# Optimization experiments

Hardware: AMD Instinct MI355X
Metric: run time of the kernel (lower is better)

The kernel has to match this reference:

```python
import jax, jax.numpy as jnp
import numpy as np

N = 50000
E = 640000
F_IN = 128
HID = 128
OUT = 64


def setup_inputs() -> dict:
    key = jax.random.key(0)
    ks = jax.random.split(key, 16)
    x = jax.random.normal(ks[0], (N, F_IN), dtype=jnp.float32)
    edge_index = jax.random.randint(ks[1], (2, E), 0, N, dtype=jnp.int64)

    def lin(k, fan_in, fan_out):
        bound = 1.0 / np.sqrt(fan_in)
        kw, kb = jax.random.split(k)
        W = jax.random.uniform(kw, (fan_in, fan_out), jnp.float32, -bound, bound)
        b = jax.random.uniform(kb, (fan_out,), jnp.float32, -bound, bound)
        return W, b

    W1, b1 = lin(ks[2], F_IN, HID)
    W2, b2 = lin(ks[3], HID, HID)
    W3, b3 = lin(ks[4], HID, HID)
    Wres, bres = lin(ks[5], F_IN, HID)
    Wlin, blin = lin(ks[6], HID, OUT)
    return {"x": x, "edge_index": edge_index,
            "W1": W1, "b1": b1, "W2": W2, "b2": b2, "W3": W3, "b3": b3,
            "Wres": Wres, "bres": bres, "Wlin": Wlin, "blin": blin}


def _gcn_norm(edge_index, n):
    # GCNConv default: add self-loops, symmetric normalization D^-1/2 (A+I) D^-1/2
    src, dst = edge_index[0], edge_index[1]
    deg = jax.ops.segment_sum(jnp.ones((edge_index.shape[1],), jnp.float32), dst,
                              num_segments=n) + 1.0  # +1 for self-loop
    dinv = jax.lax.rsqrt(deg)
    norm_e = dinv[src] * dinv[dst]          # [E] edge coefficients
    norm_self = 1.0 / deg                    # [N] self-loop coefficients
    return src, dst, norm_e, norm_self


def _gcn_conv(x, W, b, src, dst, norm_e, norm_self, n):
    h = x @ W                                # [N, F_out]
    agg = jax.ops.segment_sum(h[src] * norm_e[:, None], dst, num_segments=n)
    agg = agg + h * norm_self[:, None]       # self-loop contribution
    return agg + b


def reference(x, edge_index, W1, b1, W2, b2, W3, b3, Wres, bres, Wlin, blin):
    n = x.shape[0]
    src, dst, norm_e, norm_self = _gcn_norm(edge_index, n)
    x_res = x @ Wres + bres
    h = _gcn_conv(x, W1, b1, src, dst, norm_e, norm_self, n)
    h = jax.nn.relu(h + x_res)               # dropout is identity in eval mode
    h = _gcn_conv(h, W2, b2, src, dst, norm_e, norm_self, n)
    h = jax.nn.relu(h)
    h = _gcn_conv(h, W3, b3, src, dst, norm_e, norm_self, n)
    h = jax.nn.relu(h)
    return h @ Wlin + blin
```

## Files before the change

### kernel.cpp

```cpp
#include <hip/hip_runtime.h>

typedef unsigned short ushort_t;
typedef unsigned int uint_t;

typedef __bf16 bf16x8 __attribute__((ext_vector_type(8)));
typedef float f32x4 __attribute__((ext_vector_type(4)));

union BFU { ushort_t u; __bf16 h; };

__device__ __forceinline__ float bf2f(uint_t u) {
    union { uint_t i; float f; } v; v.i = u << 16; return v.f;
}
__device__ __forceinline__ ushort_t f2bf(float f) {
    union { float f; uint_t i; } v; v.f = f;
    uint_t r = v.i + 0x7fffu + ((v.i >> 16) & 1u);
    return (ushort_t)(r >> 16);
}
__device__ __forceinline__ float loadF(const void* p, size_t i, int isBf16) {
    return isBf16 ? bf2f((uint_t)((const ushort_t*)p)[i]) : ((const float*)p)[i];
}

struct DetectArgs {
    const void* t[11];
    int elems[11];
    const int* ei;
    int* flags;
};

__device__ __forceinline__ int detect_one(const void* p, int elems) {
    const uint_t* w = (const uint_t*)p;
    int n = elems / 2; if (n > 64) n = 64;
    int cnt = 0;
    for (int k = 0; k < n; ++k) {
        uint_t f = (w[k] >> 7) & 0xFFu;
        cnt += (f >= 100u && f <= 135u);
    }
    return (cnt * 10 >= n * 6) ? 1 : 0;
}

__global__ void k_pack(DetectArgs a,
                       ushort_t* __restrict__ Tcat, ushort_t* __restrict__ T2,
                       ushort_t* __restrict__ T3, ushort_t* __restrict__ Tl,
                       int* __restrict__ deg, int N, uint_t* __restrict__ Hz) {
    __shared__ int lflag;
    int i = blockIdx.x * blockDim.x + threadIdx.x;
    if (i < N) deg[i] = 0;
    if (blockIdx.x == 1 && threadIdx.x < 64) Hz[threadIdx.x] = 0u;
    const int SQ = 128 * 128;
    int m = (i < 4 * SQ) ? (i / SQ) : 4;
    int fid = (m == 0) ? 1 : (m == 1) ? 3 : (m == 2) ? 5 : (m == 3) ? 7 : 9;
    const void* W = a.t[fid];

    if (threadIdx.x == 0) lflag = detect_one(W, a.elems[fid]);
    if (blockIdx.x == 0 && threadIdx.x >= 64 && threadIdx.x < 75) {
        int t = threadIdx.x - 64;
        a.flags[t] = detect_one(a.t[t], a.elems[t]);
    }
    if (blockIdx.x == 0 && threadIdx.x == 75) {
        int nz = 0;
        for (int k = 0; k < 64; ++k) nz += (a.ei[2 * k + 1] != 0);
        a.flags[11] = (nz == 0) ? 1 : 0;
    }
    __syncthreads();
    int isb = lflag;

    if (i < 4 * SQ) {
        int r = i % SQ;
        int k = r / 128, f = r % 128;
        ushort_t* T = (m == 0) ? Tcat : (m == 1) ? T2 : (m == 2) ? T3 : (Tcat + SQ);
        T[f * 128 + k] = f2bf(loadF(W, (size_t)k * 128 + f, isb));
    } else if (i < 4 * SQ + 128 * 64) {
        int r = i - 4 * SQ;
        int k = r / 64, f = r % 64;
        Tl[f * 128 + k] = f2bf(loadF(W, (size_t)k * 64 + f, isb));
    }
}

__global__ void k_deg(const int* __restrict__ ei, int E, int N,
                      const int* __restrict__ flags, int* __restrict__ deg,
                      int2* __restrict__ tmp) {
    int i = blockIdx.x * blockDim.x + threadIdx.x;
    int e0 = i * 4;
    if (e0 >= E) return;
    int is64 = flags[11];
    if (e0 + 3 < E && (E & 3) == 0) {
        int d[4];
        if (is64) {
            int4 va = *(const int4*)(ei + 2 * E + 2 * e0);
            int4 vb = *(const int4*)(ei + 2 * E + 2 * e0 + 4);
            d[0] = va.x; d[1] = va.z; d[2] = vb.x; d[3] = vb.z;
        } else {
            int4 va = *(const int4*)(ei + E + e0);
            d[0] = va.x; d[1] = va.y; d[2] = va.z; d[3] = va.w;
        }
        int l[4]; bool ok[4];
#pragma unroll
        for (int k = 0; k < 4; ++k) ok[k] = (unsigned)d[k] < (unsigned)N;
#pragma unroll
        for (int k = 0; k < 4; ++k)
            l[k] = ok[k] ? atomicAdd(&deg[d[k]], 1) : 0;
        int4 t01, t23;
        t01.x = ok[0] ? d[0] : -1; t01.y = l[0];
        t01.z = ok[1] ? d[1] : -1; t01.w = l[1];
        t23.x = ok[2] ? d[2] : -1; t23.y = l[2];
        t23.z = ok[3] ? d[3] : -1; t23.w = l[3];
        *(int4*)(tmp + e0) = t01;
        *(int4*)(tmp + e0 + 2) = t23;
    } else {
        for (int e = e0; e < E && e < e0 + 4; ++e) {
            int dd = is64 ? ei[2 * E + 2 * e] : ei[E + e];
            bool ok = (unsigned)dd < (unsigned)N;
            int l = ok ? atomicAdd(&deg[dd], 1) : 0;
            tmp[e] = make_int2(ok ? dd : -1, l);
        }
    }
}


__global__ __launch_bounds__(256) void k_bsum(const int* __restrict__ deg, int n,
                                              int* __restrict__ bsum) {
    int base = blockIdx.x * 1024;
    int local = 0;
#pragma unroll
    for (int j = 0; j < 4; ++j) {
        int idx = base + threadIdx.x + j * 256;
        if (idx < n) local += deg[idx];
    }
    __shared__ int s[4];
#pragma unroll
    for (int off = 32; off; off >>= 1) local += __shfl_down(local, off, 64);
    if ((threadIdx.x & 63) == 0) s[threadIdx.x >> 6] = local;
    __syncthreads();
    if (threadIdx.x == 0) bsum[blockIdx.x] = s[0] + s[1] + s[2] + s[3];
}

__global__ __launch_bounds__(256) void k_rowptr(const int* __restrict__ deg,
                                                const int* __restrict__ bsum, int n,
                                                int* __restrict__ row_ptr,
                                                float* __restrict__ dinv) {
    __shared__ int s[256];
    __shared__ int sboff;
    int t = threadIdx.x;

    if (t < 64) {
        int v = (t < blockIdx.x) ? bsum[t] : 0;
#pragma unroll
        for (int off = 32; off; off >>= 1) v += __shfl_down(v, off, 64);
        if (t == 0) sboff = v;
    }

    int base = blockIdx.x * 1024 + t * 4;
    int v0 = (base + 0 < n) ? deg[base + 0] : 0;
    int v1 = (base + 1 < n) ? deg[base + 1] : 0;
    int v2 = (base + 2 < n) ? deg[base + 2] : 0;
    int v3 = (base + 3 < n) ? deg[base + 3] : 0;
    int tot = v0 + v1 + v2 + v3;
    s[t] = tot;
    __syncthreads();
    for (int off = 1; off < 256; off <<= 1) {
        int u = (t >= off) ? s[t - off] : 0;
        __syncthreads();
        s[t] += u;
        __syncthreads();
    }
    int run = sboff + ((t == 0) ? 0 : s[t - 1]);
    int vals[4] = {v0, v1, v2, v3};
#pragma unroll
    for (int j = 0; j < 4; ++j) {
        int idx = base + j;
        if (idx < n) {
            row_ptr[idx] = run;
            run += vals[j];
            float df = (float)vals[j] + 1.0f;
            dinv[idx] = rsqrtf(df);
        }
    }
    if (blockIdx.x == gridDim.x - 1 && t == 255) row_ptr[n] = sboff + s[255];
}

__global__ void k_scatter(const int* __restrict__ ei, int E, int N,
                          const int* __restrict__ flags,
                          const int* __restrict__ row_ptr,
                          const int2* __restrict__ tmp,
                          uint_t* __restrict__ colw) {
    int i = blockIdx.x * blockDim.x + threadIdx.x;
    int e0 = i * 4;
    if (e0 >= E) return;
    int is64 = flags[11];
    if (e0 + 3 < E && (E & 3) == 0) {
        int s[4];
        if (is64) {
            int4 sa = *(const int4*)(ei + 2 * e0);
            int4 sb = *(const int4*)(ei + 2 * e0 + 4);
            s[0] = sa.x; s[1] = sa.z; s[2] = sb.x; s[3] = sb.z;
        } else {
            int4 sa = *(const int4*)(ei + e0);
            s[0] = sa.x; s[1] = sa.y; s[2] = sa.z; s[3] = sa.w;
        }
        int4 t01 = *(const int4*)(tmp + e0);
        int4 t23 = *(const int4*)(tmp + e0 + 2);
        int d[4] = {t01.x, t01.z, t23.x, t23.z};
        int l[4] = {t01.y, t01.w, t23.y, t23.w};
        int ss[4];
#pragma unroll
        for (int k = 0; k < 4; ++k)
            ss[k] = ((unsigned)s[k] < (unsigned)N) ? s[k] : 0;
#pragma unroll
        for (int k = 0; k < 4; ++k) {
            if (d[k] >= 0)
                colw[row_ptr[d[k]] + l[k]] = (uint_t)ss[k];
        }
    } else {
        for (int e = e0; e < E && e < e0 + 4; ++e) {
            int sv = is64 ? ei[2 * e] : ei[e];
            int2 tv = tmp[e];
            if (tv.x >= 0) {
                int ssv = ((unsigned)sv < (unsigned)N) ? sv : 0;
                colw[row_ptr[tv.x] + tv.y] = (uint_t)ssv;
            }
        }
    }
}


template <int NCT>
__device__ __forceinline__ void stage_B(const ushort_t* __restrict__ WT, uint4* lds) {
    int t = threadIdx.x;
#pragma unroll
    for (int i = 0; i < NCT; ++i) {
        int g = i * 256 + t;
        uint4 v = ((const uint4*)WT)[g];
        int col = g >> 4, k8 = g & 15;
        int c = col >> 4, l16c = col & 15;
        int kk = k8 >> 2, q = k8 & 3;
        lds[((kk * NCT + c) << 6) + (q << 4) + l16c] = v;
    }
    __syncthreads();
}

__device__ __forceinline__ void load_A1(const void* __restrict__ A, int a16,
                                        int ar, int quad, bf16x8 af[4]) {
    if (a16) {
        const ushort_t* p = (const ushort_t*)A + (size_t)ar * 128 + quad * 8;
#pragma unroll
        for (int kk = 0; kk < 4; ++kk) af[kk] = *(const bf16x8*)(p + kk * 32);
    } else {
        const float* p = (const float*)A + (size_t)ar * 128 + quad * 8;
#pragma unroll
        for (int kk = 0; kk < 4; ++kk) {
            f32x4 u0 = *(const f32x4*)(p + kk * 32);
            f32x4 u1 = *(const f32x4*)(p + kk * 32 + 4);
#pragma unroll
            for (int j = 0; j < 4; ++j) {
                BFU e;
                e.u = f2bf(u0[j]); af[kk][j] = e.h;
                e.u = f2bf(u1[j]); af[kk][j + 4] = e.h;
            }
        }
    }
}

template <int NCT>
__global__ __launch_bounds__(256, 4) void k_gemm2(const void* __restrict__ A, int aFid, int aFix,
                                                  const ushort_t* __restrict__ WT,
                                                  const void* __restrict__ bias, int bFid,
                                                  void* __restrict__ C, int cFix,
                                                  int M, const int* __restrict__ flags,
                                                  const float* __restrict__ rowscale) {
    __shared__ uint4 lds[NCT * 256];
    stage_B<NCT>(WT, lds);

    const int F = NCT * 16;
    int t = threadIdx.x;
    int wave = t >> 6, lane = t & 63;
    int quad = lane >> 4, l16 = lane & 15;
    int row0 = blockIdx.x * 64 + wave * 16;

    int a16 = (aFid >= 0) ? flags[aFid] : aFix;
    int ar = row0 + l16; if (ar >= M) ar = M - 1;

    bf16x8 af[4];
    load_A1(A, a16, ar, quad, af);

    f32x4 acc[NCT];
#pragma unroll
    for (int c = 0; c < NCT; ++c) acc[c] = (f32x4){0.f, 0.f, 0.f, 0.f};

#pragma unroll
    for (int kk = 0; kk < 4; ++kk) {
#pragma unroll
        for (int c = 0; c < NCT; ++c) {
            bf16x8 b = *(const bf16x8*)&lds[((kk * NCT + c) << 6) + lane];
            acc[c] = __builtin_amdgcn_mfma_f32_16x16x32_bf16(af[kk], b, acc[c], 0, 0, 0);
        }
    }

    float rs[4];
#pragma unroll
    for (int q = 0; q < 4; ++q) {
        int row = row0 + quad * 4 + q;
        rs[q] = (rowscale && row < M) ? rowscale[row] : 1.0f;
    }

    int bf = (bias && bFid >= 0) ? flags[bFid] : 1;
#pragma unroll
    for (int c = 0; c < NCT; ++c) {
        int colg = c * 16 + l16;
        float bv = bias ? loadF(bias, colg, bf) : 0.0f;
#pragma unroll
        for (int q = 0; q < 4; ++q) {
            int row = row0 + quad * 4 + q;
            if (row < M) {
                float v = acc[c][q] * rs[q] + bv;
                if (cFix) ((ushort_t*)C)[(size_t)row * F + colg] = f2bf(v);
                else      ((float*)C)[(size_t)row * F + colg] = v;
            }
        }
    }
}

__global__ __launch_bounds__(256, 4) void k_gemm_l1(const void* __restrict__ A,
                                                    const ushort_t* __restrict__ Tcat,
                                                    const void* __restrict__ bres,
                                                    ushort_t* __restrict__ Hout,
                                                    ushort_t* __restrict__ Xres,
                                                    int M, const int* __restrict__ flags,
                                                    const float* __restrict__ dinv) {
    __shared__ uint4 lds[8 * 256];
    int t = threadIdx.x;
    int wave = t >> 6, lane = t & 63;
    int quad = lane >> 4, l16 = lane & 15;
    int row0 = blockIdx.x * 64 + wave * 16;

    int a16 = flags[0];
    int ar = row0 + l16; if (ar >= M) ar = M - 1;

    bf16x8 af[4];
    load_A1(A, a16, ar, quad, af);

    float rs[4];
#pragma unroll
    for (int q = 0; q < 4; ++q) {
        int row = row0 + quad * 4 + q;
        rs[q] = (row < M) ? dinv[row] : 1.0f;
    }

    stage_B<8>(Tcat, lds);
    {
        f32x4 acc[8];
#pragma unroll
        for (int c = 0; c < 8; ++c) acc[c] = (f32x4){0.f, 0.f, 0.f, 0.f};
#pragma unroll
        for (int kk = 0; kk < 4; ++kk) {
#pragma unroll
            for (int c = 0; c < 8; ++c) {
                bf16x8 b = *(const bf16x8*)&lds[((kk * 8 + c) << 6) + lane];
                acc[c] = __builtin_amdgcn_mfma_f32_16x16x32_bf16(af[kk], b, acc[c], 0, 0, 0);
            }
        }
#pragma unroll
        for (int c = 0; c < 8; ++c) {
            int colg = c * 16 + l16;
#pragma unroll
            for (int q = 0; q < 4; ++q) {
                int row = row0 + quad * 4 + q;
                if (row < M) Hout[(size_t)row * 128 + colg] = f2bf(acc[c][q] * rs[q]);
            }
        }
    }
    __syncthreads();

    stage_B<8>(Tcat + 128 * 128, lds);
    {
        int bf = flags[8];
        f32x4 acc[8];
#pragma unroll
        for (int c = 0; c < 8; ++c) acc[c] = (f32x4){0.f, 0.f, 0.f, 0.f};
#pragma unroll
        for (int kk = 0; kk < 4; ++kk) {
#pragma unroll
            for (int c = 0; c < 8; ++c) {
                bf16x8 b = *(const bf16x8*)&lds[((kk * 8 + c) << 6) + lane];
                acc[c] = __builtin_amdgcn_mfma_f32_16x16x32_bf16(af[kk], b, acc[c], 0, 0, 0);
            }
        }
#pragma unroll
        for (int c = 0; c < 8; ++c) {
            int colg = c * 16 + l16;
            float bv = loadF(bres, colg, bf);
#pragma unroll
            for (int q = 0; q < 4; ++q) {
                int row = row0 + quad * 4 + q;
                if (row < M) Xres[(size_t)row * 128 + colg] = f2bf(acc[c][q] + bv);
            }
        }
    }
}

__global__ __launch_bounds__(256) void k_agg(const ushort_t* __restrict__ H,
                                             const int* __restrict__ row_ptr,
                                             const uint_t* __restrict__ colw,
                                             const float* __restrict__ dinv,
                                             const void* __restrict__ bias, int bFid,
                                             const ushort_t* __restrict__ other,
                                             ushort_t* __restrict__ Out,
                                             int n, const int* __restrict__ flags) {
    int node = (blockIdx.x * blockDim.x + threadIdx.x) >> 6;
    if (node >= n) return;
    int lane = threadIdx.x & 63;
    int f = lane * 2;

    size_t nidx = (size_t)node * 128 + f;

    uint_t hv = *(const uint_t*)(H + nidx);
    float a0 = bf2f(hv & 0xffffu);
    float a1 = bf2f(hv >> 16);

    int beg = row_ptr[node], end = row_ptr[node + 1];
    for (int bs = beg; bs < end; bs += 64) {
        int rem = end - bs;
        int nb = (rem < 64) ? rem : 64;
        int c = (lane < nb) ? (int)colw[bs + lane] : n;

        for (int j = 0; j < nb; j += 16) {
            int si[16]; uint_t vi[16];
#pragma unroll
            for (int q = 0; q < 16; ++q) si[q] = __shfl(c, j + q, 64);
#pragma unroll
            for (int q = 0; q < 16; ++q)
                vi[q] = *(const uint_t*)(H + (size_t)si[q] * 128 + f);
#pragma unroll
            for (int q = 0; q < 16; ++q) {
                a0 += bf2f(vi[q] & 0xffffu);
                a1 += bf2f(vi[q] >> 16);
            }
        }
    }

    float dv = dinv[node];
    int bfm = flags[bFid];
    float a0o = fmaf(a0, dv, loadF(bias, f, bfm));
    float a1o = fmaf(a1, dv, loadF(bias, f + 1, bfm));
    if (other) {
        uint_t ov = *(const uint_t*)(other + nidx);
        a0o += bf2f(ov & 0xffffu);
        a1o += bf2f(ov >> 16);
    }
    a0o = fmaxf(a0o, 0.0f);
    a1o = fmaxf(a1o, 0.0f);
    *(uint_t*)(Out + nidx) = (uint_t)f2bf(a0o) | ((uint_t)f2bf(a1o) << 16);
}


extern "C" void kernel_launch(void* const* d_in, const int* in_sizes, int n_in,
                              void* d_out, int out_size, void* d_ws, size_t ws_size,
                              hipStream_t stream) {
    const int N = in_sizes[0] / 128;
    const int E = in_sizes[1] / 2;

    const void* x  = d_in[0];
    const int*  ei = (const int*)d_in[1];

    char* ws = (char*)d_ws;
    size_t used = 0;
    auto alloc = [&](size_t bytes) {
        char* p = ws + used;
        used += (bytes + 255) & ~(size_t)255;
        return p;
    };

    int*   flags   = (int*)alloc(64 * 4);
    int*   deg     = (int*)alloc((size_t)N * 4);
    int*   row_ptr = (int*)alloc((size_t)(N + 1) * 4);
    float* dinv    = (float*)alloc((size_t)N * 4);
    int2*  tmp     = (int2*)alloc((size_t)E * 8);
    uint_t* colw   = (uint_t*)alloc((size_t)E * 4);
    int*   bsum    = (int*)alloc(256 * 4);
    ushort_t* Tcat = (ushort_t*)alloc(256 * 128 * 2);
    ushort_t* T2   = (ushort_t*)alloc(128 * 128 * 2);
    ushort_t* T3   = (ushort_t*)alloc(128 * 128 * 2);
    ushort_t* Tlin = (ushort_t*)alloc(128 * 64 * 2);

    ushort_t* Hbuf = (ushort_t*)alloc((size_t)(N + 1) * 128 * 2);
    ushort_t* Act1 = (ushort_t*)alloc((size_t)N * 128 * 2);
    ushort_t* Act2 = (ushort_t*)alloc((size_t)N * 128 * 2);
    ushort_t* Xres = (ushort_t*)alloc((size_t)N * 128 * 2);

    if (used > ws_size) return;

    DetectArgs da;
    for (int i = 0; i < 11; ++i) { da.t[i] = d_in[i == 0 ? 0 : i + 1]; da.elems[i] = in_sizes[i == 0 ? 0 : i + 1]; }
    da.ei = ei;
    da.flags = flags;

    const int B = 256;
    int gE4   = ((E + 3) / 4 + B - 1) / B;
    int gPack = (4 * 128 * 128 + 128 * 64) / B;
    int gGemm = (N + 63) / 64;
    int gAgg  = (N + 3) / 4;
    int nb    = (N + 1023) / 1024;

    uint_t* Hz = (uint_t*)(Hbuf + (size_t)N * 128);

    k_pack<<<gPack, B, 0, stream>>>(da, Tcat, T2, T3, Tlin, deg, N, Hz);
    k_deg<<<gE4, B, 0, stream>>>(ei, E, N, flags, deg, tmp);
    k_bsum<<<nb, B, 0, stream>>>(deg, N, bsum);
    k_rowptr<<<nb, B, 0, stream>>>(deg, bsum, N, row_ptr, dinv);
    k_scatter<<<gE4, B, 0, stream>>>(ei, E, N, flags, row_ptr, tmp, colw);

    k_gemm_l1<<<gGemm, B, 0, stream>>>(x, Tcat, d_in[9], Hbuf, Xres, N, flags, dinv);
    k_agg<<<gAgg, B, 0, stream>>>(Hbuf, row_ptr, colw, dinv, d_in[3], 2,
                                  Xres, Act1, N, flags);

    k_gemm2<8><<<gGemm, B, 0, stream>>>(Act1, -1, 1, T2, nullptr, -1, Hbuf, 1, N, flags, dinv);
    k_agg<<<gAgg, B, 0, stream>>>(Hbuf, row_ptr, colw, dinv, d_in[5], 4,
                                  nullptr, Act2, N, flags);

    k_gemm2<8><<<gGemm, B, 0, stream>>>(Act2, -1, 1, T3, nullptr, -1, Hbuf, 1, N, flags, dinv);
    k_agg<<<gAgg, B, 0, stream>>>(Hbuf, row_ptr, colw, dinv, d_in[7], 6,
                                  nullptr, Act1, N, flags);

    k_gemm2<4><<<gGemm, B, 0, stream>>>(Act1, -1, 1, Tlin, d_in[11], 10,
                                        d_out, 0, N, flags, nullptr);
}
```

Measured before the change: 284.2 us.

## Split aggregation features across four blocks and edges across wave quarters

The aggregation kernel now gives each node's 128 features to four blocks of 32 features each. Within a wave, each quarter processes a different subset of the neighbors, and the partial sums are combined with xor shuffles. Index loads, residual loads and output stores use nontemporal hints. The aim is more parallelism and shorter per-wave dependency chains on low-degree nodes, at the cost of four times as many blocks and narrower 64-byte gather segments per row.

```diff
diff --git a/kernel.cpp b/kernel.cpp
--- a/kernel.cpp
+++ b/kernel.cpp
@@ -405,50 +405,59 @@
                                              const ushort_t* __restrict__ other,
                                              ushort_t* __restrict__ Out,
                                              int n, const int* __restrict__ flags) {
-    int node = (blockIdx.x * blockDim.x + threadIdx.x) >> 6;
+    int s = blockIdx.x & 3;
+    int node = (blockIdx.x >> 2) * 4 + (threadIdx.x >> 6);
     if (node >= n) return;
     int lane = threadIdx.x & 63;
-    int f = lane * 2;
-
+    int e4 = lane >> 4;
+    int fl = lane & 15;
+    int f = s * 32 + fl * 2;
     size_t nidx = (size_t)node * 128 + f;
 
-    uint_t hv = *(const uint_t*)(H + nidx);
-    float a0 = bf2f(hv & 0xffffu);
-    float a1 = bf2f(hv >> 16);
-
     int beg = row_ptr[node], end = row_ptr[node + 1];
+    float a0 = 0.f, a1 = 0.f;
+
     for (int bs = beg; bs < end; bs += 64) {
         int rem = end - bs;
         int nb = (rem < 64) ? rem : 64;
-        int c = (lane < nb) ? (int)colw[bs + lane] : n;
+        int c = (lane < nb) ? (int)__builtin_nontemporal_load(&colw[bs + lane]) : n;
 
         for (int j = 0; j < nb; j += 16) {
-            int si[16]; uint_t vi[16];
-#pragma unroll
-            for (int q = 0; q < 16; ++q) si[q] = __shfl(c, j + q, 64);
-#pragma unroll
-            for (int q = 0; q < 16; ++q)
-                vi[q] = *(const uint_t*)(H + (size_t)si[q] * 128 + f);
-#pragma unroll
-            for (int q = 0; q < 16; ++q) {
-                a0 += bf2f(vi[q] & 0xffffu);
-                a1 += bf2f(vi[q] >> 16);
-            }
-        }
-    }
-
-    float dv = dinv[node];
-    int bfm = flags[bFid];
-    float a0o = fmaf(a0, dv, loadF(bias, f, bfm));
-    float a1o = fmaf(a1, dv, loadF(bias, f + 1, bfm));
-    if (other) {
-        uint_t ov = *(const uint_t*)(other + nidx);
-        a0o += bf2f(ov & 0xffffu);
-        a1o += bf2f(ov >> 16);
-    }
-    a0o = fmaxf(a0o, 0.0f);
-    a1o = fmaxf(a1o, 0.0f);
-    *(uint_t*)(Out + nidx) = (uint_t)f2bf(a0o) | ((uint_t)f2bf(a1o) << 16);
+            int ce[4]; uint_t v[4];
+#pragma unroll
+            for (int q = 0; q < 4; ++q) ce[q] = __shfl(c, j + q * 4 + e4, 64);
+#pragma unroll
+            for (int q = 0; q < 4; ++q)
+                v[q] = *(const uint_t*)(H + (size_t)ce[q] * 128 + f);
+#pragma unroll
+            for (int q = 0; q < 4; ++q) {
+                a0 += bf2f(v[q] & 0xffffu);
+                a1 += bf2f(v[q] >> 16);
+            }
+        }
+    }
+
+    a0 += __shfl_xor(a0, 16, 64); a1 += __shfl_xor(a1, 16, 64);
+    a0 += __shfl_xor(a0, 32, 64); a1 += __shfl_xor(a1, 32, 64);
+
+    if (e4 == 0) {
+        uint_t hv = *(const uint_t*)(H + nidx);
+        a0 += bf2f(hv & 0xffffu);
+        a1 += bf2f(hv >> 16);
+        float dv = dinv[node];
+        int bfm = flags[bFid];
+        float a0o = fmaf(a0, dv, loadF(bias, f, bfm));
+        float a1o = fmaf(a1, dv, loadF(bias, f + 1, bfm));
+        if (other) {
+            uint_t ov = __builtin_nontemporal_load((const uint_t*)(other + nidx));
+            a0o += bf2f(ov & 0xffffu);
+            a1o += bf2f(ov >> 16);
+        }
+        a0o = fmaxf(a0o, 0.0f);
+        a1o = fmaxf(a1o, 0.0f);
+        __builtin_nontemporal_store((uint_t)f2bf(a0o) | ((uint_t)f2bf(a1o) << 16),
+                                    (uint_t*)(Out + nidx));
+    }
 }
 
 
@@ -497,7 +506,7 @@
     int gE4   = ((E + 3) / 4 + B - 1) / B;
     int gPack = (4 * 128 * 128 + 128 * 64) / B;
     int gGemm = (N + 63) / 64;
-    int gAgg  = (N + 3) / 4;
+    int gAgg  = ((N + 3) / 4) * 4;
     int nb    = (N + 1023) / 1024;
 
     uint_t* Hz = (uint_t*)(Hbuf + (size_t)N * 128);
```

After: 422.0 us. +48.5%, slower.

## Fuse neighbor aggregation with following GEMM via LDS-staged activation tiles

Applied to the files above, without the earlier changes.

Merges each aggregation kernel with the next layer's dense GEMM. Each wave aggregates 16 nodes serially, writes the bf16 activations into an LDS tile, then runs MFMA against the staged weights. The bf16 activation round trip through global memory and three launches go away, and ping-pong H buffers get zeroed padding rows. In exchange the grid drops from one wave per node to one wave per 16 nodes, which cuts parallelism for the latency-bound gather, and occupancy falls with the extra LDS and the launch bound lowered to 3.

```diff
diff --git a/kernel.cpp b/kernel.cpp
--- a/kernel.cpp
+++ b/kernel.cpp
@@ -41,11 +41,15 @@
 __global__ void k_pack(DetectArgs a,
                        ushort_t* __restrict__ Tcat, ushort_t* __restrict__ T2,
                        ushort_t* __restrict__ T3, ushort_t* __restrict__ Tl,
-                       int* __restrict__ deg, int N, uint_t* __restrict__ Hz) {
+                       int* __restrict__ deg, int N,
+                       uint_t* __restrict__ HzA, uint_t* __restrict__ HzB) {
     __shared__ int lflag;
     int i = blockIdx.x * blockDim.x + threadIdx.x;
     if (i < N) deg[i] = 0;
-    if (blockIdx.x == 1 && threadIdx.x < 64) Hz[threadIdx.x] = 0u;
+    if (blockIdx.x == 1 && threadIdx.x < 128) {
+        uint_t* Hz = (threadIdx.x < 64) ? HzA : HzB;
+        Hz[threadIdx.x & 63] = 0u;
+    }
     const int SQ = 128 * 128;
     int m = (i < 4 * SQ) ? (i / SQ) : 4;
     int fid = (m == 0) ? 1 : (m == 1) ? 3 : (m == 2) ? 5 : (m == 3) ? 7 : 9;
@@ -260,65 +264,6 @@
     }
 }
 
-template <int NCT>
-__global__ __launch_bounds__(256, 4) void k_gemm2(const void* __restrict__ A, int aFid, int aFix,
-                                                  const ushort_t* __restrict__ WT,
-                                                  const void* __restrict__ bias, int bFid,
-                                                  void* __restrict__ C, int cFix,
-                                                  int M, const int* __restrict__ flags,
-                                                  const float* __restrict__ rowscale) {
-    __shared__ uint4 lds[NCT * 256];
-    stage_B<NCT>(WT, lds);
-
-    const int F = NCT * 16;
-    int t = threadIdx.x;
-    int wave = t >> 6, lane = t & 63;
-    int quad = lane >> 4, l16 = lane & 15;
-    int row0 = blockIdx.x * 64 + wave * 16;
-
-    int a16 = (aFid >= 0) ? flags[aFid] : aFix;
-    int ar = row0 + l16; if (ar >= M) ar = M - 1;
-
-    bf16x8 af[4];
-    load_A1(A, a16, ar, quad, af);
-
-    f32x4 acc[NCT];
-#pragma unroll
-    for (int c = 0; c < NCT; ++c) acc[c] = (f32x4){0.f, 0.f, 0.f, 0.f};
-
-#pragma unroll
-    for (int kk = 0; kk < 4; ++kk) {
-#pragma unroll
-        for (int c = 0; c < NCT; ++c) {
-            bf16x8 b = *(const bf16x8*)&lds[((kk * NCT + c) << 6) + lane];
-            acc[c] = __builtin_amdgcn_mfma_f32_16x16x32_bf16(af[kk], b, acc[c], 0, 0, 0);
-        }
-    }
-
-    float rs[4];
-#pragma unroll
-    for (int q = 0; q < 4; ++q) {
-        int row = row0 + quad * 4 + q;
-        rs[q] = (rowscale && row < M) ? rowscale[row] : 1.0f;
-    }
-
-    int bf = (bias && bFid >= 0) ? flags[bFid] : 1;
-#pragma unroll
-    for (int c = 0; c < NCT; ++c) {
-        int colg = c * 16 + l16;
-        float bv = bias ? loadF(bias, colg, bf) : 0.0f;
-#pragma unroll
-        for (int q = 0; q < 4; ++q) {
-            int row = row0 + quad * 4 + q;
-            if (row < M) {
-                float v = acc[c][q] * rs[q] + bv;
-                if (cFix) ((ushort_t*)C)[(size_t)row * F + colg] = f2bf(v);
-                else      ((float*)C)[(size_t)row * F + colg] = v;
-            }
-        }
-    }
-}
-
 __global__ __launch_bounds__(256, 4) void k_gemm_l1(const void* __restrict__ A,
                                                     const ushort_t* __restrict__ Tcat,
                                                     const void* __restrict__ bres,
@@ -397,58 +342,123 @@
     }
 }
 
-__global__ __launch_bounds__(256) void k_agg(const ushort_t* __restrict__ H,
-                                             const int* __restrict__ row_ptr,
-                                             const uint_t* __restrict__ colw,
-                                             const float* __restrict__ dinv,
-                                             const void* __restrict__ bias, int bFid,
-                                             const ushort_t* __restrict__ other,
-                                             ushort_t* __restrict__ Out,
-                                             int n, const int* __restrict__ flags) {
-    int node = (blockIdx.x * blockDim.x + threadIdx.x) >> 6;
-    if (node >= n) return;
-    int lane = threadIdx.x & 63;
+template <int NCT, int CF32>
+__global__ __launch_bounds__(256, 3) void k_fused(const ushort_t* __restrict__ H,
+                                                  const int* __restrict__ row_ptr,
+                                                  const uint_t* __restrict__ colw,
+                                                  const float* __restrict__ dinv,
+                                                  const void* __restrict__ bagg, int baggFid,
+                                                  const ushort_t* __restrict__ other,
+                                                  const ushort_t* __restrict__ WT,
+                                                  const void* __restrict__ bgemm, int bgFid,
+                                                  void* __restrict__ C,
+                                                  int n, const int* __restrict__ flags) {
+    __shared__ uint4 lds_w[NCT * 256];
+    __shared__ uint_t lds_act[4 * 16 * 68];
+
+    stage_B<NCT>(WT, lds_w);
+
+    int t = threadIdx.x;
+    int wave = t >> 6, lane = t & 63;
     int f = lane * 2;
-
-    size_t nidx = (size_t)node * 128 + f;
-
-    uint_t hv = *(const uint_t*)(H + nidx);
-    float a0 = bf2f(hv & 0xffffu);
-    float a1 = bf2f(hv >> 16);
-
-    int beg = row_ptr[node], end = row_ptr[node + 1];
-    for (int bs = beg; bs < end; bs += 64) {
-        int rem = end - bs;
-        int nb = (rem < 64) ? rem : 64;
-        int c = (lane < nb) ? (int)colw[bs + lane] : n;
-
-        for (int j = 0; j < nb; j += 16) {
-            int si[16]; uint_t vi[16];
-#pragma unroll
-            for (int q = 0; q < 16; ++q) si[q] = __shfl(c, j + q, 64);
-#pragma unroll
-            for (int q = 0; q < 16; ++q)
-                vi[q] = *(const uint_t*)(H + (size_t)si[q] * 128 + f);
-#pragma unroll
-            for (int q = 0; q < 16; ++q) {
-                a0 += bf2f(vi[q] & 0xffffu);
-                a1 += bf2f(vi[q] >> 16);
-            }
-        }
-    }
-
-    float dv = dinv[node];
-    int bfm = flags[bFid];
-    float a0o = fmaf(a0, dv, loadF(bias, f, bfm));
-    float a1o = fmaf(a1, dv, loadF(bias, f + 1, bfm));
-    if (other) {
-        uint_t ov = *(const uint_t*)(other + nidx);
-        a0o += bf2f(ov & 0xffffu);
-        a1o += bf2f(ov >> 16);
-    }
-    a0o = fmaxf(a0o, 0.0f);
-    a1o = fmaxf(a1o, 0.0f);
-    *(uint_t*)(Out + nidx) = (uint_t)f2bf(a0o) | ((uint_t)f2bf(a1o) << 16);
+    int row0 = blockIdx.x * 64 + wave * 16;
+    uint_t* act = lds_act + wave * (16 * 68);
+    int bfm = flags[baggFid];
+
+    for (int i = 0; i < 16; ++i) {
+        int node = row0 + i;
+        int nd = (node < n) ? node : (n - 1);
+        int beg = row_ptr[nd], end = row_ptr[nd + 1];
+
+        uint_t hv = *(const uint_t*)(H + (size_t)nd * 128 + f);
+        float a0 = bf2f(hv & 0xffffu);
+        float a1 = bf2f(hv >> 16);
+
+        for (int bs = beg; bs < end; bs += 64) {
+            int rem = end - bs;
+            int nb = (rem < 64) ? rem : 64;
+            int c = (lane < nb) ? (int)colw[bs + lane] : n;
+
+            for (int j = 0; j < nb; j += 16) {
+                int si[16]; uint_t vi[16];
+#pragma unroll
+                for (int q = 0; q < 16; ++q) si[q] = __shfl(c, j + q, 64);
+#pragma unroll
+                for (int q = 0; q < 16; ++q)
+                    vi[q] = *(const uint_t*)(H + (size_t)si[q] * 128 + f);
+#pragma unroll
+                for (int q = 0; q < 16; ++q) {
+                    a0 += bf2f(vi[q] & 0xffffu);
+                    a1 += bf2f(vi[q] >> 16);
+                }
+            }
+        }
+
+        float dv = dinv[nd];
+        float a0o = fmaf(a0, dv, loadF(bagg, f, bfm));
+        float a1o = fmaf(a1, dv, loadF(bagg, f + 1, bfm));
+        if (other) {
+            uint_t ov = *(const uint_t*)(other + (size_t)nd * 128 + f);
+            a0o += bf2f(ov & 0xffffu);
+            a1o += bf2f(ov >> 16);
+        }
+        a0o = fmaxf(a0o, 0.0f);
+        a1o = fmaxf(a1o, 0.0f);
+        act[i * 68 + lane] = (uint_t)f2bf(a0o) | ((uint_t)f2bf(a1o) << 16);
+    }
+
+    int quad = lane >> 4, l16 = lane & 15;
+
+    bf16x8 af[4];
+#pragma unroll
+    for (int kk = 0; kk < 4; ++kk)
+        af[kk] = *(const bf16x8*)&act[l16 * 68 + kk * 16 + quad * 4];
+
+    f32x4 acc[NCT];
+#pragma unroll
+    for (int c = 0; c < NCT; ++c) acc[c] = (f32x4){0.f, 0.f, 0.f, 0.f};
+
+#pragma unroll
+    for (int kk = 0; kk < 4; ++kk) {
+#pragma unroll
+        for (int c = 0; c < NCT; ++c) {
+            bf16x8 b = *(const bf16x8*)&lds_w[((kk * NCT + c) << 6) + lane];
+            acc[c] = __builtin_amdgcn_mfma_f32_16x16x32_bf16(af[kk], b, acc[c], 0, 0, 0);
+        }
+    }
+
+    const int F = NCT * 16;
+    if (CF32) {
+        int bg = (bgemm) ? flags[bgFid] : 1;
+#pragma unroll
+        for (int c = 0; c < NCT; ++c) {
+            int colg = c * 16 + l16;
+            float bv = bgemm ? loadF(bgemm, colg, bg) : 0.0f;
+#pragma unroll
+            for (int q = 0; q < 4; ++q) {
+                int row = row0 + quad * 4 + q;
+                if (row < n)
+                    ((float*)C)[(size_t)row * F + colg] = acc[c][q] + bv;
+            }
+        }
+    } else {
+        float rs[4];
+#pragma unroll
+        for (int q = 0; q < 4; ++q) {
+            int row = row0 + quad * 4 + q;
+            rs[q] = (row < n) ? dinv[row] : 1.0f;
+        }
+#pragma unroll
+        for (int c = 0; c < NCT; ++c) {
+            int colg = c * 16 + l16;
+#pragma unroll
+            for (int q = 0; q < 4; ++q) {
+                int row = row0 + quad * 4 + q;
+                if (row < n)
+                    ((ushort_t*)C)[(size_t)row * F + colg] = f2bf(acc[c][q] * rs[q]);
+            }
+        }
+    }
 }
 
 
@@ -481,9 +491,8 @@
     ushort_t* T3   = (ushort_t*)alloc(128 * 128 * 2);
     ushort_t* Tlin = (ushort_t*)alloc(128 * 64 * 2);
 
-    ushort_t* Hbuf = (ushort_t*)alloc((size_t)(N + 1) * 128 * 2);
-    ushort_t* Act1 = (ushort_t*)alloc((size_t)N * 128 * 2);
-    ushort_t* Act2 = (ushort_t*)alloc((size_t)N * 128 * 2);
+    ushort_t* Ha   = (ushort_t*)alloc((size_t)(N + 1) * 128 * 2);
+    ushort_t* Hb   = (ushort_t*)alloc((size_t)(N + 1) * 128 * 2);
     ushort_t* Xres = (ushort_t*)alloc((size_t)N * 128 * 2);
 
     if (used > ws_size) return;
@@ -497,29 +506,25 @@
     int gE4   = ((E + 3) / 4 + B - 1) / B;
     int gPack = (4 * 128 * 128 + 128 * 64) / B;
     int gGemm = (N + 63) / 64;
-    int gAgg  = (N + 3) / 4;
     int nb    = (N + 1023) / 1024;
 
-    uint_t* Hz = (uint_t*)(Hbuf + (size_t)N * 128);
-
-    k_pack<<<gPack, B, 0, stream>>>(da, Tcat, T2, T3, Tlin, deg, N, Hz);
+    uint_t* HzA = (uint_t*)(Ha + (size_t)N * 128);
+    uint_t* HzB = (uint_t*)(Hb + (size_t)N * 128);
+
+    k_pack<<<gPack, B, 0, stream>>>(da, Tcat, T2, T3, Tlin, deg, N, HzA, HzB);
     k_deg<<<gE4, B, 0, stream>>>(ei, E, N, flags, deg, tmp);
     k_bsum<<<nb, B, 0, stream>>>(deg, N, bsum);
     k_rowptr<<<nb, B, 0, stream>>>(deg, bsum, N, row_ptr, dinv);
     k_scatter<<<gE4, B, 0, stream>>>(ei, E, N, flags, row_ptr, tmp, colw);
 
-    k_gemm_l1<<<gGemm, B, 0, stream>>>(x, Tcat, d_in[9], Hbuf, Xres, N, flags, dinv);
-    k_agg<<<gAgg, B, 0, stream>>>(Hbuf, row_ptr, colw, dinv, d_in[3], 2,
-                                  Xres, Act1, N, flags);
-
-    k_gemm2<8><<<gGemm, B, 0, stream>>>(Act1, -1, 1, T2, nullptr, -1, Hbuf, 1, N, flags, dinv);
-    k_agg<<<gAgg, B, 0, stream>>>(Hbuf, row_ptr, colw, dinv, d_in[5], 4,
-                                  nullptr, Act2, N, flags);
-
-    k_gemm2<8><<<gGemm, B, 0, stream>>>(Act2, -1, 1, T3, nullptr, -1, Hbuf, 1, N, flags, dinv);
-    k_agg<<<gAgg, B, 0, stream>>>(Hbuf, row_ptr, colw, dinv, d_in[7], 6,
-                                  nullptr, Act1, N, flags);
-
-    k_gemm2<4><<<gGemm, B, 0, stream>>>(Act1, -1, 1, Tlin, d_in[11], 10,
-                                        d_out, 0, N, flags, nullptr);
-}
+    k_gemm_l1<<<gGemm, B, 0, stream>>>(x, Tcat, d_in[9], Ha, Xres, N, flags, dinv);
+
+    k_fused<8, 0><<<gGemm, B, 0, stream>>>(Ha, row_ptr, colw, dinv, d_in[3], 2,
+                                           Xres, T2, nullptr, -1, Hb, N, flags);
+
+    k_fused<8, 0><<<gGemm, B, 0, stream>>>(Hb, row_ptr, colw, dinv, d_in[5], 4,
+                                           nullptr, T3, nullptr, -1, Ha, N, flags);
+
+    k_fused<4, 1><<<gGemm, B, 0, stream>>>(Ha, row_ptr, colw, dinv, d_in[7], 6,
+                                           nullptr, Tlin, d_in[11], 10, d_out, N, flags);
+}
```

Result: slower. 348.6 us (+22.7%).

## Split each aggregation wave into two half-waves gathering different neighbors with wider loads

Applied to the files above, without the earlier changes.

Restructures the CSR gather so each 64-lane wave handles two neighbor rows at once: each 32-lane half loads 4 bf16 features (8 bytes) per lane for alternating neighbors, and the halves are combined with a cross-half shuffle at the end. Neighbor indices are read as wave-uniform scalar loads of 16 at a time instead of a per-lane load plus shuffles. The goal is to raise memory-level parallelism and cut shuffle overhead in the bandwidth-bound gather. The column buffer is padded so the 16-wide index reads past the end stay in bounds, and for low-degree nodes some slots point at a dummy row n, which adds wasted loads.

```diff
diff --git a/kernel.cpp b/kernel.cpp
--- a/kernel.cpp
+++ b/kernel.cpp
@@ -408,47 +408,68 @@
     int node = (blockIdx.x * blockDim.x + threadIdx.x) >> 6;
     if (node >= n) return;
     int lane = threadIdx.x & 63;
-    int f = lane * 2;
-
-    size_t nidx = (size_t)node * 128 + f;
-
-    uint_t hv = *(const uint_t*)(H + nidx);
-    float a0 = bf2f(hv & 0xffffu);
-    float a1 = bf2f(hv >> 16);
-
-    int beg = row_ptr[node], end = row_ptr[node + 1];
-    for (int bs = beg; bs < end; bs += 64) {
-        int rem = end - bs;
-        int nb = (rem < 64) ? rem : 64;
-        int c = (lane < nb) ? (int)colw[bs + lane] : n;
-
-        for (int j = 0; j < nb; j += 16) {
-            int si[16]; uint_t vi[16];
-#pragma unroll
-            for (int q = 0; q < 16; ++q) si[q] = __shfl(c, j + q, 64);
-#pragma unroll
-            for (int q = 0; q < 16; ++q)
-                vi[q] = *(const uint_t*)(H + (size_t)si[q] * 128 + f);
-#pragma unroll
-            for (int q = 0; q < 16; ++q) {
-                a0 += bf2f(vi[q] & 0xffffu);
-                a1 += bf2f(vi[q] >> 16);
-            }
-        }
-    }
-
-    float dv = dinv[node];
-    int bfm = flags[bFid];
-    float a0o = fmaf(a0, dv, loadF(bias, f, bfm));
-    float a1o = fmaf(a1, dv, loadF(bias, f + 1, bfm));
-    if (other) {
-        uint_t ov = *(const uint_t*)(other + nidx);
-        a0o += bf2f(ov & 0xffffu);
-        a1o += bf2f(ov >> 16);
-    }
-    a0o = fmaxf(a0o, 0.0f);
-    a1o = fmaxf(a1o, 0.0f);
-    *(uint_t*)(Out + nidx) = (uint_t)f2bf(a0o) | ((uint_t)f2bf(a1o) << 16);
+    int half = lane >> 5;
+    int l32 = lane & 31;
+    int f = l32 * 4;
+
+    int beg = __builtin_amdgcn_readfirstlane(row_ptr[node]);
+    int end = __builtin_amdgcn_readfirstlane(row_ptr[node + 1]);
+
+    float a0 = 0.f, a1 = 0.f, a2 = 0.f, a3 = 0.f;
+
+    for (int b = beg; b < end; b += 16) {
+        int rem = end - b;
+        const uint_t* cw = colw + b;
+        int cs[16];
+#pragma unroll
+        for (int q = 0; q < 16; ++q) {
+            int cv = (int)cw[q];
+            cs[q] = (q < rem) ? cv : n;
+        }
+#pragma unroll
+        for (int q = 0; q < 8; ++q) {
+            int row = half ? cs[2 * q + 1] : cs[2 * q];
+            uint2 v = *(const uint2*)(H + (size_t)row * 128 + f);
+            a0 += bf2f(v.x & 0xffffu);
+            a1 += bf2f(v.x >> 16);
+            a2 += bf2f(v.y & 0xffffu);
+            a3 += bf2f(v.y >> 16);
+        }
+    }
+
+    a0 += __shfl_xor(a0, 32, 64);
+    a1 += __shfl_xor(a1, 32, 64);
+    a2 += __shfl_xor(a2, 32, 64);
+    a3 += __shfl_xor(a3, 32, 64);
+
+    if (half == 0) {
+        size_t nidx = (size_t)node * 128 + f;
+        uint2 hv = *(const uint2*)(H + nidx);
+        a0 += bf2f(hv.x & 0xffffu);
+        a1 += bf2f(hv.x >> 16);
+        a2 += bf2f(hv.y & 0xffffu);
+        a3 += bf2f(hv.y >> 16);
+
+        float dv = dinv[node];
+        int bfm = flags[bFid];
+        float o0 = fmaf(a0, dv, loadF(bias, f + 0, bfm));
+        float o1 = fmaf(a1, dv, loadF(bias, f + 1, bfm));
+        float o2 = fmaf(a2, dv, loadF(bias, f + 2, bfm));
+        float o3 = fmaf(a3, dv, loadF(bias, f + 3, bfm));
+        if (other) {
+            uint2 ov = *(const uint2*)(other + nidx);
+            o0 += bf2f(ov.x & 0xffffu);
+            o1 += bf2f(ov.x >> 16);
+            o2 += bf2f(ov.y & 0xffffu);
+            o3 += bf2f(ov.y >> 16);
+        }
+        o0 = fmaxf(o0, 0.0f); o1 = fmaxf(o1, 0.0f);
+        o2 = fmaxf(o2, 0.0f); o3 = fmaxf(o3, 0.0f);
+        uint2 outv;
+        outv.x = (uint_t)f2bf(o0) | ((uint_t)f2bf(o1) << 16);
+        outv.y = (uint_t)f2bf(o2) | ((uint_t)f2bf(o3) << 16);
+        *(uint2*)(Out + nidx) = outv;
+    }
 }
 
 
@@ -474,7 +495,7 @@
     int*   row_ptr = (int*)alloc((size_t)(N + 1) * 4);
     float* dinv    = (float*)alloc((size_t)N * 4);
     int2*  tmp     = (int2*)alloc((size_t)E * 8);
-    uint_t* colw   = (uint_t*)alloc((size_t)E * 4);
+    uint_t* colw   = (uint_t*)alloc((size_t)E * 4 + 256);
     int*   bsum    = (int*)alloc(256 * 4);
     ushort_t* Tcat = (ushort_t*)alloc(256 * 128 * 2);
     ushort_t* T2   = (ushort_t*)alloc(128 * 128 * 2);
```

Result: slower. 409.9 us (+44.2%).
